# Kernel optimization log

Hardware: AMD Instinct MI355X
Metric: run time of the kernel (lower is better)

The kernel has to match this reference:

```python
import jax, jax.numpy as jnp
import numpy as np

N = 100000   # nodes
E = 640000   # edges
DIN = 128
H = 128
DOUT = 64
EPS = 1e-5   # BatchNorm eps


def setup_inputs() -> dict:
    key = jax.random.key(0)
    ks = jax.random.split(key, 20)
    x = jax.random.normal(ks[0], (N, DIN), jnp.float32)
    edge_index = jax.random.randint(ks[1], (2, E), 0, N, dtype=jnp.int64)
    ricci_curvature = jax.random.normal(ks[2], (E,), jnp.float32)
    s = 0.05
    W1 = jax.random.normal(ks[3], (DIN, H), jnp.float32) * s
    b1 = jnp.zeros((H,), jnp.float32)
    Wm = jax.random.normal(ks[4], (H, H), jnp.float32) * s
    bm = jnp.zeros((H,), jnp.float32)
    W2 = jax.random.normal(ks[5], (H, DOUT), jnp.float32) * s
    b2 = jnp.zeros((DOUT,), jnp.float32)
    def bn_params(k, d):
        k1, k2, k3, k4 = jax.random.split(k, 4)
        g = jax.random.uniform(k1, (d,), jnp.float32) + 0.5
        b = jax.random.normal(k2, (d,), jnp.float32) * 0.1
        m = jax.random.normal(k3, (d,), jnp.float32) * 0.1
        v = jax.random.uniform(k4, (d,), jnp.float32) + 0.5
        return g, b, m, v
    bn1_g, bn1_b, bn1_m, bn1_v = bn_params(ks[6], DIN)
    bnm_g, bnm_b, bnm_m, bnm_v = bn_params(ks[7], H)
    bn2_g, bn2_b, bn2_m, bn2_v = bn_params(ks[8], H)
    return dict(x=x, edge_index=edge_index, percent=50,
                ricci_curvature=ricci_curvature,
                W1=W1, b1=b1, Wm=Wm, bm=bm, W2=W2, b2=b2,
                bn1_g=bn1_g, bn1_b=bn1_b, bn1_m=bn1_m, bn1_v=bn1_v,
                bnm_g=bnm_g, bnm_b=bnm_b, bnm_m=bnm_m, bnm_v=bnm_v,
                bn2_g=bn2_g, bn2_b=bn2_b, bn2_m=bn2_m, bn2_v=bn2_v)


def _bn_eval(x, g, b, m, v):
    # BatchNorm1d in eval mode: running stats
    return (x - m) * (g * jax.lax.rsqrt(v + EPS)) + b


def _gcn_conv(x, W, bias, src, dst):
    # PyG GCNConv: x' = D^{-1/2} (A+I) D^{-1/2} (x W) + b
    h = x @ W                              # [N, F_out]
    loops = jnp.arange(N, dtype=src.dtype)
    s = jnp.concatenate([src, loops])      # [E+N]
    d = jnp.concatenate([dst, loops])
    deg = jax.ops.segment_sum(jnp.ones_like(d, h.dtype), d, num_segments=N)
    dinv = jax.lax.rsqrt(deg)              # deg >= 1 (self loops)
    norm = dinv[s] * dinv[d]               # [E+N]
    out = jax.ops.segment_sum(h[s] * norm[:, None], d, num_segments=N)
    return out + bias


def reference(x, edge_index, percent, ricci_curvature,
              W1, b1, Wm, bm, W2, b2,
              bn1_g, bn1_b, bn1_m, bn1_v,
              bnm_g, bnm_b, bnm_m, bnm_v,
              bn2_g, bn2_b, bn2_m, bn2_v):
    # Eval mode: no edge sampling (percent / ricci_curvature unused),
    # dropout inactive, BN uses running statistics.
    src, dst = edge_index[0], edge_index[1]
    h = _bn_eval(x, bn1_g, bn1_b, bn1_m, bn1_v)
    h = jax.nn.relu(_gcn_conv(h, W1, b1, src, dst))
    res1 = h
    h = _bn_eval(h, bnm_g, bnm_b, bnm_m, bnm_v)
    h = jax.nn.relu(_gcn_conv(h, Wm, bm, src, dst))
    res2 = h
    h = _bn_eval(h, bn2_g, bn2_b, bn2_m, bn2_v)
    out = _gcn_conv(h, W2, b2, src, dst)
    return (out, res1, res2)
```

## Files before the change

kernel.cpp:

```cpp
#include <hip/hip_runtime.h>

#define N_NODES 100000
#define N_EDGES 640000
#define DIN 128
#define HDIM 128
#define DOUT 64

typedef __attribute__((ext_vector_type(4))) float f32x4;
typedef __attribute__((ext_vector_type(8))) short bf16x8;

__device__ inline unsigned short f2bf(float x) {
    unsigned u = __float_as_uint(x);
    unsigned r = (u + 0x7fffu + ((u >> 16) & 1u)) >> 16;
    return (unsigned short)r;
}
__device__ inline void unpack2(unsigned u, float& f0, float& f1) {
    f0 = __uint_as_float(u << 16);
    f1 = __uint_as_float(u & 0xffff0000u);
}

struct PrepPtrs {
    const float *g[3], *b[3], *m[3], *v[3];
    const float *W[3];
    float *tW[3];
    unsigned short *wt[3];
};

__global__ void combo_prep_kernel(const int* __restrict__ ei, int* __restrict__ cnt,
                                  int* __restrict__ rank, int ne, int gE, PrepPtrs p) {
    int bid = blockIdx.x, tid = threadIdx.x;
    if (bid < gE) {
        int e = bid * 256 + tid;
        if (e < ne) rank[e] = atomicAdd(&cnt[ei[ne + e]], 1);
        return;
    }
    if (bid < gE + 3) {
        __shared__ float sh_s[128];
        int l = bid - gE;
        if (tid < 128) {
            float s  = p.g[l][tid] * rsqrtf(p.v[l][tid] + 1e-5f);
            sh_s[tid] = p.b[l][tid] - p.m[l][tid] * s;
        }
        __syncthreads();
        int cout = (l == 2) ? DOUT : HDIM;
        if (tid < cout) {
            float acc = 0.f;
            for (int k = 0; k < 128; ++k) acc += sh_s[k] * p.W[l][k * cout + tid];
            p.tW[l][tid] = acc;
        }
        return;
    }
    {
        int idx0 = bid - gE - 3;
        int l = idx0 >> 6;
        int cout = (l == 2) ? DOUT : HDIM;
        int idx = (idx0 & 63) * 256 + tid;
        if (idx >= 128 * cout) return;
        int k = idx / cout, c = idx % cout;
        float sc = p.g[l][k] * rsqrtf(p.v[l][k] + 1e-5f);
        p.wt[l][c * 128 + k] = f2bf(p.W[l][idx] * sc);
    }
}

__global__ void scan_block_kernel(const int* __restrict__ cnt, int* __restrict__ off,
                                  int* __restrict__ bsums, int n) {
    __shared__ int sm[1024];
    int tid = threadIdx.x;
    int i = blockIdx.x * 1024 + tid;
    int v = (i < n) ? cnt[i] : 0;
    sm[tid] = v;
    __syncthreads();
    for (int d = 1; d < 1024; d <<= 1) {
        int t = (tid >= d) ? sm[tid - d] : 0;
        __syncthreads();
        sm[tid] += t;
        __syncthreads();
    }
    if (i < n) off[i] = sm[tid] - v;
    if (tid == 1023) bsums[blockIdx.x] = sm[1023];
}

__global__ void scan_add_kernel(int* __restrict__ off, const int* __restrict__ bsums,
                                const int* __restrict__ cnt, float* __restrict__ dinv,
                                int2* __restrict__ rng, int n, int nb) {
    __shared__ int red[4];
    int tid = threadIdx.x;
    int b = blockIdx.x >> 2;
    int pv = (tid < b) ? bsums[tid] : 0;
    #pragma unroll
    for (int o = 32; o > 0; o >>= 1) pv += __shfl_down(pv, o);
    if ((tid & 63) == 0) red[tid >> 6] = pv;
    __syncthreads();
    int base = red[0] + red[1] + red[2] + red[3];
    int i = blockIdx.x * 256 + tid;
    if (i < n) {
        int o = off[i] + base;
        int c = cnt[i];
        off[i] = o;
        rng[i] = make_int2(o, o + c);
        dinv[i] = rsqrtf((float)c + 1.0f);
    }
}

__global__ void fill_csr_kernel(const int* __restrict__ ei, const float* __restrict__ dinv,
                                const int* __restrict__ off, const int* __restrict__ rank,
                                int2* __restrict__ csr, int ne) {
    int e = blockIdx.x * 256 + threadIdx.x;
    if (e < ne) {
        int s = ei[e], d = ei[ne + e];
        int2 ent;
        ent.x = s;
        ent.y = __float_as_int(dinv[s] * dinv[d]);
        csr[off[d] + rank[e]] = ent;
    }
}

template<int COUT>
__global__ __launch_bounds__(256) void gemm_mfma_kernel(
    const float* __restrict__ X, const unsigned short* __restrict__ Wt,
    const float* __restrict__ tW, unsigned short* __restrict__ T, int nrows)
{
    constexpr int LDT = 136;
    __shared__ unsigned short xs[64 * LDT];
    __shared__ unsigned short ws[COUT * LDT];

    int tid  = threadIdx.x;
    int wave = tid >> 6, lane = tid & 63;
    int row0 = blockIdx.x * 64;

    {
        const uint4* src = (const uint4*)Wt;
        #pragma unroll
        for (int it = 0; it < COUT / 16; ++it) {
            int idx = tid + it * 256;
            int r = idx >> 4, c8 = idx & 15;
            uint4 v = src[idx];
            *(uint4*)&ws[r * LDT + c8 * 8] = v;
        }
    }
    {
        const float4* X4 = (const float4*)X;
        #pragma unroll
        for (int it = 0; it < 8; ++it) {
            int idx = tid + it * 256;
            int r = idx >> 5, c4 = idx & 31;
            int row = row0 + r;
            float4 v = make_float4(0.f, 0.f, 0.f, 0.f);
            if (row < nrows) v = X4[(size_t)row * 32 + c4];
            ushort4 o;
            o.x = f2bf(v.x); o.y = f2bf(v.y); o.z = f2bf(v.z); o.w = f2bf(v.w);
            *(ushort4*)&xs[r * LDT + c4 * 4] = o;
        }
    }
    __syncthreads();

    constexpr int NT = COUT / 16;
    f32x4 acc[NT];
    #pragma unroll
    for (int t = 0; t < NT; ++t) acc[t] = (f32x4)(0.f);

    int arow = wave * 16 + (lane & 15);
    int khi  = (lane >> 4) * 8;

    #pragma unroll
    for (int kk = 0; kk < 4; ++kk) {
        bf16x8 a = *(const bf16x8*)&xs[arow * LDT + kk * 32 + khi];
        #pragma unroll
        for (int t = 0; t < NT; ++t) {
            bf16x8 b = *(const bf16x8*)&ws[(t * 16 + (lane & 15)) * LDT + kk * 32 + khi];
            acc[t] = __builtin_amdgcn_mfma_f32_16x16x32_bf16(a, b, acc[t], 0, 0, 0);
        }
    }

    int crow0 = (lane >> 4) * 4;
    int ccol  = lane & 15;
    #pragma unroll
    for (int t = 0; t < NT; ++t) {
        int col = t * 16 + ccol;
        float tw = tW[col];
        #pragma unroll
        for (int r = 0; r < 4; ++r) {
            int row = row0 + wave * 16 + crow0 + r;
            if (row < nrows)
                T[(size_t)row * COUT + col] = f2bf(acc[t][r] + tw);
        }
    }
}

#define GACC(vv, cc)                                                     \
    {                                                                    \
        float _f0, _f1;                                                  \
        unpack2(vv.x, _f0, _f1); acc[0] += _f0 * cc; acc[1] += _f1 * cc; \
        unpack2(vv.y, _f0, _f1); acc[2] += _f0 * cc; acc[3] += _f1 * cc; \
        unpack2(vv.z, _f0, _f1); acc[4] += _f0 * cc; acc[5] += _f1 * cc; \
        unpack2(vv.w, _f0, _f1); acc[6] += _f0 * cc; acc[7] += _f1 * cc; \
    }

template<int COUT, bool RELU>
__global__ __launch_bounds__(256) void gather_kernel(
    const unsigned short* __restrict__ T, const float* __restrict__ dinv,
    const int2* __restrict__ rng, const int2* __restrict__ csr,
    const float* __restrict__ bias, float* __restrict__ out, int n)
{
    constexpr int LPN = COUT / 8;
    int tid = blockIdx.x * 256 + threadIdx.x;
    int node = tid / LPN, lane = tid % LPN;
    if (node >= n) return;

    const uint4* T4 = (const uint4*)T;
    float di  = dinv[node];
    float cf0 = di * di;

    float acc[8];
    {
        uint4 tv = T4[(size_t)node * LPN + lane];
        float f[8];
        unpack2(tv.x, f[0], f[1]); unpack2(tv.y, f[2], f[3]);
        unpack2(tv.z, f[4], f[5]); unpack2(tv.w, f[6], f[7]);
        float4 b0 = ((const float4*)bias)[lane * 2];
        float4 b1 = ((const float4*)bias)[lane * 2 + 1];
        acc[0] = f[0] * cf0 + b0.x; acc[1] = f[1] * cf0 + b0.y;
        acc[2] = f[2] * cf0 + b0.z; acc[3] = f[3] * cf0 + b0.w;
        acc[4] = f[4] * cf0 + b1.x; acc[5] = f[5] * cf0 + b1.y;
        acc[6] = f[6] * cf0 + b1.z; acc[7] = f[7] * cf0 + b1.w;
    }

    int2 r = rng[node];
    int e = r.x, en = r.y;
    for (; e + 3 < en; e += 4) {
        int2 p0 = csr[e], p1 = csr[e + 1], p2 = csr[e + 2], p3 = csr[e + 3];
        uint4 v0 = T4[(size_t)p0.x * LPN + lane];
        uint4 v1 = T4[(size_t)p1.x * LPN + lane];
        uint4 v2 = T4[(size_t)p2.x * LPN + lane];
        uint4 v3 = T4[(size_t)p3.x * LPN + lane];
        float c0 = __int_as_float(p0.y), c1 = __int_as_float(p1.y);
        float c2 = __int_as_float(p2.y), c3 = __int_as_float(p3.y);
        GACC(v0, c0); GACC(v1, c1); GACC(v2, c2); GACC(v3, c3);
    }
    if (e + 1 < en) {
        int2 p0 = csr[e], p1 = csr[e + 1];
        uint4 v0 = T4[(size_t)p0.x * LPN + lane];
        uint4 v1 = T4[(size_t)p1.x * LPN + lane];
        float c0 = __int_as_float(p0.y), c1 = __int_as_float(p1.y);
        GACC(v0, c0); GACC(v1, c1);
        e += 2;
    }
    if (e < en) {
        int2 p0 = csr[e];
        uint4 v0 = T4[(size_t)p0.x * LPN + lane];
        float c0 = __int_as_float(p0.y);
        GACC(v0, c0);
    }

    if (RELU) {
        #pragma unroll
        for (int j = 0; j < 8; ++j) acc[j] = fmaxf(acc[j], 0.f);
    }
    float4* O4 = (float4*)out;
    float4 o0, o1;
    o0.x = acc[0]; o0.y = acc[1]; o0.z = acc[2]; o0.w = acc[3];
    o1.x = acc[4]; o1.y = acc[5]; o1.z = acc[6]; o1.w = acc[7];
    O4[(size_t)node * LPN * 2 + lane * 2]     = o0;
    O4[(size_t)node * LPN * 2 + lane * 2 + 1] = o1;
}

extern "C" void kernel_launch(void* const* d_in, const int* in_sizes, int n_in,
                              void* d_out, int out_size, void* d_ws, size_t ws_size,
                              hipStream_t stream) {
    const float* x   = (const float*)d_in[0];
    const int*   ei  = (const int*)d_in[1];
    const float* W1  = (const float*)d_in[4];
    const float* b1  = (const float*)d_in[5];
    const float* Wm  = (const float*)d_in[6];
    const float* bm  = (const float*)d_in[7];
    const float* W2  = (const float*)d_in[8];
    const float* b2  = (const float*)d_in[9];

    float* out  = (float*)d_out;
    float* res1 = out + (size_t)N_NODES * DOUT;
    float* res2 = res1 + (size_t)N_NODES * HDIM;

    unsigned short* T   = (unsigned short*)d_ws;
    unsigned short* wt1 = T + (size_t)N_NODES * HDIM;
    unsigned short* wtm = wt1 + 128 * HDIM;
    unsigned short* wt2 = wtm + 128 * HDIM;
    float* dinv = (float*)(wt2 + DOUT * 128);
    float* tW1  = dinv + N_NODES;
    float* tWm  = tW1 + 128;
    float* tW2  = tWm + 128;
    int*   cnt   = (int*)(tW2 + 64);
    int*   off   = cnt + N_NODES;
    int*   bsums = off + N_NODES;
    int*   rank  = bsums + 128;
    int2*  rng   = (int2*)(rank + N_EDGES);
    int2*  csr   = (int2*)(rng + N_NODES);

    int gN = (N_NODES + 255) / 256;
    int gE = (N_EDGES + 255) / 256;
    int gT = (N_NODES + 63) / 64;
    int nb = (N_NODES + 1023) / 1024;

    PrepPtrs p;
    p.g[0] = (const float*)d_in[10]; p.b[0] = (const float*)d_in[11];
    p.m[0] = (const float*)d_in[12]; p.v[0] = (const float*)d_in[13];
    p.g[1] = (const float*)d_in[14]; p.b[1] = (const float*)d_in[15];
    p.m[1] = (const float*)d_in[16]; p.v[1] = (const float*)d_in[17];
    p.g[2] = (const float*)d_in[18]; p.b[2] = (const float*)d_in[19];
    p.m[2] = (const float*)d_in[20]; p.v[2] = (const float*)d_in[21];
    p.W[0] = W1; p.W[1] = Wm; p.W[2] = W2;
    p.tW[0] = tW1; p.tW[1] = tWm; p.tW[2] = tW2;
    p.wt[0] = wt1; p.wt[1] = wtm; p.wt[2] = wt2;

    hipMemsetAsync(cnt, 0, N_NODES * sizeof(int), stream);
    combo_prep_kernel<<<gE + 3 + 192, 256, 0, stream>>>(ei, cnt, rank, N_EDGES, gE, p);
    scan_block_kernel<<<nb, 1024, 0, stream>>>(cnt, off, bsums, N_NODES);
    scan_add_kernel<<<gN, 256, 0, stream>>>(off, bsums, cnt, dinv, rng, N_NODES, nb);
    fill_csr_kernel<<<gE, 256, 0, stream>>>(ei, dinv, off, rank, csr, N_EDGES);

    int gG128 = (N_NODES * 16 + 255) / 256;
    int gG64  = (N_NODES * 8 + 255) / 256;

    gemm_mfma_kernel<128><<<gT, 256, 0, stream>>>(x, wt1, tW1, T, N_NODES);
    gather_kernel<128, true><<<gG128, 256, 0, stream>>>(T, dinv, rng, csr, b1, res1, N_NODES);

    gemm_mfma_kernel<128><<<gT, 256, 0, stream>>>(res1, wtm, tWm, T, N_NODES);
    gather_kernel<128, true><<<gG128, 256, 0, stream>>>(T, dinv, rng, csr, bm, res2, N_NODES);

    gemm_mfma_kernel<64><<<gT, 256, 0, stream>>>(res2, wt2, tW2, T, N_NODES);
    gather_kernel<64, false><<<gG64, 256, 0, stream>>>(T, dinv, rng, csr, b2, out, N_NODES);
}
```

Measured before the change: 223.3 us.

## Fuse neighbor gather with following layer's MFMA GEMM per 64-row tile

```diff
diff --git a/kernel.cpp b/kernel.cpp
--- a/kernel.cpp
+++ b/kernel.cpp
@@ -196,6 +196,125 @@
         unpack2(vv.w, _f0, _f1); acc[6] += _f0 * cc; acc[7] += _f1 * cc; \
     }
 
+template<int COUT>
+__global__ __launch_bounds__(1024, 8) void fused_gather_gemm_kernel(
+    const unsigned short* __restrict__ Tin, const float* __restrict__ dinv,
+    const int2* __restrict__ rng, const int2* __restrict__ csr,
+    const float* __restrict__ bias, float* __restrict__ res,
+    const unsigned short* __restrict__ Wt, const float* __restrict__ tW,
+    unsigned short* __restrict__ Tout, int n)
+{
+    constexpr int LDT = 136;
+    __shared__ unsigned short xs[64 * LDT];
+    __shared__ unsigned short ws[COUT * LDT];
+
+    int tid  = threadIdx.x;
+    int row0 = blockIdx.x * 64;
+
+    {
+        const uint4* src = (const uint4*)Wt;
+        #pragma unroll
+        for (int it = 0; it < COUT / 64; ++it) {
+            int idx = tid + it * 1024;
+            int r = idx >> 4, c8 = idx & 15;
+            uint4 v = src[idx];
+            *(uint4*)&ws[r * LDT + c8 * 8] = v;
+        }
+    }
+
+    int lr   = tid >> 4;
+    int node = row0 + lr;
+    int lane = tid & 15;
+    {
+        float acc[8];
+        if (node < n) {
+            const uint4* T4 = (const uint4*)Tin;
+            float di  = dinv[node];
+            float cf0 = di * di;
+            {
+                uint4 tv = T4[(size_t)node * 16 + lane];
+                float f[8];
+                unpack2(tv.x, f[0], f[1]); unpack2(tv.y, f[2], f[3]);
+                unpack2(tv.z, f[4], f[5]); unpack2(tv.w, f[6], f[7]);
+                float4 b0 = ((const float4*)bias)[lane * 2];
+                float4 b1 = ((const float4*)bias)[lane * 2 + 1];
+                acc[0] = f[0] * cf0 + b0.x; acc[1] = f[1] * cf0 + b0.y;
+                acc[2] = f[2] * cf0 + b0.z; acc[3] = f[3] * cf0 + b0.w;
+                acc[4] = f[4] * cf0 + b1.x; acc[5] = f[5] * cf0 + b1.y;
+                acc[6] = f[6] * cf0 + b1.z; acc[7] = f[7] * cf0 + b1.w;
+            }
+            int2 r = rng[node];
+            int e = r.x, en = r.y;
+            for (; e + 1 < en; e += 2) {
+                int2 p0 = csr[e], p1 = csr[e + 1];
+                uint4 v0 = T4[(size_t)p0.x * 16 + lane];
+                uint4 v1 = T4[(size_t)p1.x * 16 + lane];
+                float c0 = __int_as_float(p0.y), c1 = __int_as_float(p1.y);
+                GACC(v0, c0); GACC(v1, c1);
+            }
+            if (e < en) {
+                int2 p0 = csr[e];
+                uint4 v0 = T4[(size_t)p0.x * 16 + lane];
+                float c0 = __int_as_float(p0.y);
+                GACC(v0, c0);
+            }
+            #pragma unroll
+            for (int j = 0; j < 8; ++j) acc[j] = fmaxf(acc[j], 0.f);
+
+            float4 o0, o1;
+            o0.x = acc[0]; o0.y = acc[1]; o0.z = acc[2]; o0.w = acc[3];
+            o1.x = acc[4]; o1.y = acc[5]; o1.z = acc[6]; o1.w = acc[7];
+            ((float4*)res)[(size_t)node * 32 + lane * 2]     = o0;
+            ((float4*)res)[(size_t)node * 32 + lane * 2 + 1] = o1;
+        } else {
+            #pragma unroll
+            for (int j = 0; j < 8; ++j) acc[j] = 0.f;
+        }
+        ushort4 h0, h1;
+        h0.x = f2bf(acc[0]); h0.y = f2bf(acc[1]); h0.z = f2bf(acc[2]); h0.w = f2bf(acc[3]);
+        h1.x = f2bf(acc[4]); h1.y = f2bf(acc[5]); h1.z = f2bf(acc[6]); h1.w = f2bf(acc[7]);
+        *(ushort4*)&xs[lr * LDT + lane * 8]     = h0;
+        *(ushort4*)&xs[lr * LDT + lane * 8 + 4] = h1;
+    }
+    __syncthreads();
+
+    constexpr int TPW = (COUT / 16) / 4;
+    int wave = tid >> 6, lane64 = tid & 63;
+    int rt  = wave & 3;
+    int ct0 = (wave >> 2) * TPW;
+
+    f32x4 acc2[TPW];
+    #pragma unroll
+    for (int t = 0; t < TPW; ++t) acc2[t] = (f32x4)(0.f);
+
+    int arow = rt * 16 + (lane64 & 15);
+    int khi  = (lane64 >> 4) * 8;
+
+    #pragma unroll
+    for (int kk = 0; kk < 4; ++kk) {
+        bf16x8 a = *(const bf16x8*)&xs[arow * LDT + kk * 32 + khi];
+        #pragma unroll
+        for (int t = 0; t < TPW; ++t) {
+            bf16x8 b = *(const bf16x8*)&ws[((ct0 + t) * 16 + (lane64 & 15)) * LDT + kk * 32 + khi];
+            acc2[t] = __builtin_amdgcn_mfma_f32_16x16x32_bf16(a, b, acc2[t], 0, 0, 0);
+        }
+    }
+
+    int crow0 = (lane64 >> 4) * 4;
+    int ccol  = lane64 & 15;
+    #pragma unroll
+    for (int t = 0; t < TPW; ++t) {
+        int col = (ct0 + t) * 16 + ccol;
+        float tw = tW[col];
+        #pragma unroll
+        for (int r = 0; r < 4; ++r) {
+            int row = row0 + rt * 16 + crow0 + r;
+            if (row < n)
+                Tout[(size_t)row * COUT + col] = f2bf(acc2[t][r] + tw);
+        }
+    }
+}
+
 template<int COUT, bool RELU>
 __global__ __launch_bounds__(256) void gather_kernel(
     const unsigned short* __restrict__ T, const float* __restrict__ dinv,
@@ -281,7 +400,8 @@
     float* res2 = res1 + (size_t)N_NODES * HDIM;
 
     unsigned short* T   = (unsigned short*)d_ws;
-    unsigned short* wt1 = T + (size_t)N_NODES * HDIM;
+    unsigned short* T2  = T + (size_t)N_NODES * HDIM;
+    unsigned short* wt1 = T2 + (size_t)N_NODES * HDIM;
     unsigned short* wtm = wt1 + 128 * HDIM;
     unsigned short* wt2 = wtm + 128 * HDIM;
     float* dinv = (float*)(wt2 + DOUT * 128);
@@ -317,15 +437,14 @@
     scan_add_kernel<<<gN, 256, 0, stream>>>(off, bsums, cnt, dinv, rng, N_NODES, nb);
     fill_csr_kernel<<<gE, 256, 0, stream>>>(ei, dinv, off, rank, csr, N_EDGES);
 
-    int gG128 = (N_NODES * 16 + 255) / 256;
-    int gG64  = (N_NODES * 8 + 255) / 256;
-
     gemm_mfma_kernel<128><<<gT, 256, 0, stream>>>(x, wt1, tW1, T, N_NODES);
-    gather_kernel<128, true><<<gG128, 256, 0, stream>>>(T, dinv, rng, csr, b1, res1, N_NODES);
-
-    gemm_mfma_kernel<128><<<gT, 256, 0, stream>>>(res1, wtm, tWm, T, N_NODES);
-    gather_kernel<128, true><<<gG128, 256, 0, stream>>>(T, dinv, rng, csr, bm, res2, N_NODES);
-
-    gemm_mfma_kernel<64><<<gT, 256, 0, stream>>>(res2, wt2, tW2, T, N_NODES);
-    gather_kernel<64, false><<<gG64, 256, 0, stream>>>(T, dinv, rng, csr, b2, out, N_NODES);
-}
+
+    fused_gather_gemm_kernel<128><<<gT, 1024, 0, stream>>>(
+        T, dinv, rng, csr, b1, res1, wtm, tWm, T2, N_NODES);
+
+    fused_gather_gemm_kernel<64><<<gT, 1024, 0, stream>>>(
+        T2, dinv, rng, csr, bm, res2, wt2, tW2, T, N_NODES);
+
+    gather_kernel<64, false><<<(N_NODES * 8 + 255) / 256, 256, 0, stream>>>(
+        T, dinv, rng, csr, b2, out, N_NODES);
+}
```

Result: faster. 200.8 us (-10.1%).
